# Performance work log

Measured on AMD Instinct MI355X. Metric: run time of the kernel, lower is better.

## Reference

```python
import jax, jax.numpy as jnp
import numpy as np

N_EMBD = 2048
QKV_EMBD = 2048
N_HEAD = 32
N_KV_HEAD = 8
HEAD_DIM = QKV_EMBD // N_HEAD  # 64
GROUPS = N_HEAD // N_KV_HEAD   # 4
ROPE_THETA = 10000.0
SCALE = float(np.sqrt(HEAD_DIM))


def setup_inputs() -> dict:
    key = jax.random.key(0)
    ks = jax.random.split(key, 12)
    B, S = 2, 2048
    inp = {
        "query": jax.random.normal(ks[0], (B, S, N_EMBD), jnp.float32),
        "key": jax.random.normal(ks[1], (B, S, N_EMBD), jnp.float32),
        "value": jax.random.normal(ks[2], (B, S, N_EMBD), jnp.float32),
        "mask": jnp.ones((B, S), dtype=bool),
        "Wq": jax.random.normal(ks[3], (QKV_EMBD, N_EMBD), jnp.float32) * 0.02,
        "bq": jnp.zeros((QKV_EMBD,), jnp.float32),
        "Wk": jax.random.normal(ks[4], (N_KV_HEAD * HEAD_DIM, N_EMBD), jnp.float32) * 0.02,
        "bk": jnp.zeros((N_KV_HEAD * HEAD_DIM,), jnp.float32),
        "Wv": jax.random.normal(ks[5], (N_KV_HEAD * HEAD_DIM, N_EMBD), jnp.float32) * 0.02,
        "bv": jnp.zeros((N_KV_HEAD * HEAD_DIM,), jnp.float32),
        "Wo": jax.random.normal(ks[6], (N_EMBD, QKV_EMBD), jnp.float32) * 0.02,
        "bo": jnp.zeros((N_EMBD,), jnp.float32),
    }
    return inp


def _rotate_half(x):
    d = x.shape[-1] // 2
    return jnp.concatenate([-x[..., d:], x[..., :d]], axis=-1)


def _rope_cos_sin(seq_len, dtype):
    # rope_factor == 1.0 -> no NTK adjustment; is_causal -> position_ids = arange
    inv_freq = 1.0 / (ROPE_THETA ** (jnp.arange(0, HEAD_DIM, 2, dtype=jnp.float32) / HEAD_DIM))
    pos = jnp.arange(seq_len, dtype=jnp.float32)
    freqs = jnp.einsum("i,j->ij", pos, inv_freq)           # [S, D/2]
    emb = jnp.concatenate([freqs, freqs], axis=-1)          # [S, D]
    return jnp.cos(emb).astype(dtype)[None, None], jnp.sin(emb).astype(dtype)[None, None]


def reference(query, key, value, mask, Wq, bq, Wk, bk, Wv, bv, Wo, bo):
    B, S, _ = query.shape
    Q = (query @ Wq.T + bq).reshape(B, S, N_HEAD, HEAD_DIM).transpose(0, 2, 1, 3)      # [B,H,S,D]
    K = (key @ Wk.T + bk).reshape(B, S, N_KV_HEAD, HEAD_DIM).transpose(0, 2, 1, 3)     # [B,KV,S,D]
    V = (value @ Wv.T + bv).reshape(B, S, N_KV_HEAD, HEAD_DIM).transpose(0, 2, 1, 3)

    cos, sin = _rope_cos_sin(S, Q.dtype)
    Q = Q * cos + _rotate_half(Q) * sin
    K = K * cos + _rotate_half(K) * sin

    # interleaved GQA repeat: each kv head serves GROUPS consecutive query heads
    K = jnp.repeat(K, GROUPS, axis=1)  # [B,H,S,D]
    V = jnp.repeat(V, GROUPS, axis=1)

    attn = jnp.einsum("bhqd,bhkd->bhqk", Q, K)              # [B,H,S,S]
    causal = jnp.tril(jnp.ones((S, S), dtype=bool))
    full_mask = mask[:, None, None, :] & causal[None, None]  # [B,1,S,S]
    attn = jnp.where(full_mask, attn, jnp.finfo(attn.dtype).min)
    attn_weights = jax.nn.softmax(attn / SCALE, axis=-1)     # dropout p=0 (eval)
    out = jnp.einsum("bhqk,bhkd->bhqd", attn_weights, V)
    out = out.transpose(0, 2, 1, 3).reshape(B, S, QKV_EMBD)
    return out @ Wo.T + bo
```

## Files before the change

### kernel.cpp

```cpp
#include <hip/hip_runtime.h>
#include <hip/hip_bf16.h>
#include <cmath>

#define NE   2048
#define NH   32
#define NKV  8
#define HD   64
#define SEQ  2048
#define NB   2

typedef __attribute__((ext_vector_type(4))) float f32x4;
typedef __attribute__((ext_vector_type(16))) float f32x16;
typedef __attribute__((ext_vector_type(8))) short bf16x8;
typedef __attribute__((ext_vector_type(4))) short bf16x4;

typedef const __attribute__((address_space(1))) void cgvoid;
typedef __attribute__((address_space(3))) void lvoid;

#define QSCALE 0.18033688011112042f

__device__ __forceinline__ short f2bf(float f) {
  union { float f; unsigned u; } v; v.f = f;
  unsigned r = v.u + 0x7fffu + ((v.u >> 16) & 1u);
  return (short)(r >> 16);
}

__device__ __forceinline__ unsigned cvt_pk_bf16(float a, float b) {
  unsigned r;
  asm("v_cvt_pk_bf16_f32 %0, %1, %2" : "=v"(r) : "v"(a), "v"(b));
  return r;
}

__global__ __launch_bounds__(256) void cvt_all(
    const float* __restrict__ s0, short* __restrict__ d0,
    const float* __restrict__ s1, short* __restrict__ d1,
    const float* __restrict__ s2, short* __restrict__ d2,
    const float* __restrict__ s3, short* __restrict__ d3,
    const float* __restrict__ s4, short* __restrict__ d4,
    const float* __restrict__ s5, short* __restrict__ d5,
    const float* __restrict__ s6, short* __restrict__ d6)
{
  int idx = blockIdx.x * 256 + threadIdx.x;
  const float* s; short* d; int rel;
  if      (idx < 1048576) { s = s0; d = d0; rel = idx; }
  else if (idx < 2097152) { s = s1; d = d1; rel = idx - 1048576; }
  else if (idx < 3145728) { s = s2; d = d2; rel = idx - 2097152; }
  else if (idx < 3670016) { s = s3; d = d3; rel = idx - 3145728; }
  else if (idx < 3801088) { s = s4; d = d4; rel = idx - 3670016; }
  else if (idx < 3932160) { s = s5; d = d5; rel = idx - 3801088; }
  else                    { s = s6; d = d6; rel = idx - 3932160; }
  size_t off = (size_t)rel * 8;
  f32x4 a = *(const f32x4*)(s + off);
  f32x4 b = *(const f32x4*)(s + off + 4);
  bf16x8 o;
  #pragma unroll
  for (int j = 0; j < 4; ++j) { o[j] = f2bf(a[j]); o[4 + j] = f2bf(b[j]); }
  *(bf16x8*)(d + off) = o;
}

template<int EPI>
__device__ __forceinline__ void gemm_body(
    short* As, short* Ws, int m0, int n0,
    const short* __restrict__ A, const short* __restrict__ W,
    const float* __restrict__ bias, void* __restrict__ Cout,
    int N, int K)
{
  const int t = threadIdx.x, lane = t & 63, w = t >> 6;
  const int lr = lane & 15, lg = lane >> 4;
  const int wm = (w >> 1) * 64, wn = (w & 1) * 64;

  const int sr = t >> 2, sc = (t & 3) * 8;
  const short* gA0 = A + (size_t)(m0 + sr) * K + sc;
  const short* gA1 = A + (size_t)(m0 + 64 + sr) * K + sc;
  const short* gW0 = W + (size_t)(n0 + sr) * K + sc;
  const short* gW1 = W + (size_t)(n0 + 64 + sr) * K + sc;
  short* lA0 = As + t * 8;
  short* lA1 = As + 2048 + t * 8;
  short* lW0 = Ws + t * 8;
  short* lW1 = Ws + 2048 + t * 8;

  f32x4 acc[4][4];
  #pragma unroll
  for (int i = 0; i < 4; ++i)
    #pragma unroll
    for (int j = 0; j < 4; ++j) acc[i][j] = (f32x4){0.f, 0.f, 0.f, 0.f};

  for (int k0 = 0; k0 < K; k0 += 32) {
    __builtin_amdgcn_global_load_lds((cgvoid*)(gA0 + k0), (lvoid*)lA0, 16, 0, 0);
    __builtin_amdgcn_global_load_lds((cgvoid*)(gA1 + k0), (lvoid*)lA1, 16, 0, 0);
    __builtin_amdgcn_global_load_lds((cgvoid*)(gW0 + k0), (lvoid*)lW0, 16, 0, 0);
    __builtin_amdgcn_global_load_lds((cgvoid*)(gW1 + k0), (lvoid*)lW1, 16, 0, 0);
    __syncthreads();
    bf16x8 af[4], wf[4];
    #pragma unroll
    for (int mf = 0; mf < 4; ++mf)
      af[mf] = *(const bf16x8*)(As + (wm + mf * 16 + lr) * 32 + lg * 8);
    #pragma unroll
    for (int nf = 0; nf < 4; ++nf)
      wf[nf] = *(const bf16x8*)(Ws + (wn + nf * 16 + lr) * 32 + lg * 8);
    #pragma unroll
    for (int mf = 0; mf < 4; ++mf)
      #pragma unroll
      for (int nf = 0; nf < 4; ++nf)
        acc[mf][nf] = __builtin_amdgcn_mfma_f32_16x16x32_bf16(af[mf], wf[nf], acc[mf][nf], 0, 0, 0);
    __syncthreads();
  }

  if (EPI == 0) {
    float* C = (float*)Cout;
    #pragma unroll
    for (int mf = 0; mf < 4; ++mf)
      #pragma unroll
      for (int nf = 0; nf < 4; ++nf)
        #pragma unroll
        for (int i = 0; i < 4; ++i) {
          int m = m0 + wm + mf * 16 + lg * 4 + i;
          int n = n0 + wn + nf * 16 + lr;
          C[(size_t)m * N + n] = acc[mf][nf][i] + bias[n];
        }
  } else if (EPI == 1) {
    short* C = (short*)Cout;
    #pragma unroll
    for (int mf = 0; mf < 4; ++mf)
      #pragma unroll
      for (int nf = 0; nf < 4; ++nf) {
        int n = n0 + wn + nf * 16 + lr;
        int kv = n >> 6, d = n & 63;
        int mb = m0 + wm + mf * 16 + lg * 4;
        int b = mb >> 11, s = mb & (SEQ - 1);
        bf16x4 pb;
        #pragma unroll
        for (int i = 0; i < 4; ++i) pb[i] = f2bf(acc[mf][nf][i] + bias[n]);
        *(bf16x4*)(C + (((size_t)b * NKV + kv) * HD + d) * SEQ + s) = pb;
      }
  } else {
    const int HN = (EPI == 2) ? NH : NKV;
    short* C = (short*)Cout;
    #pragma unroll
    for (int mf = 0; mf < 4; ++mf)
      #pragma unroll
      for (int nf2 = 0; nf2 < 2; ++nf2)
        #pragma unroll
        for (int i = 0; i < 4; ++i) {
          int m = m0 + wm + mf * 16 + lg * 4 + i;
          int b = m >> 11, s = m & (SEQ - 1);
          int n1 = n0 + wn + nf2 * 16 + lr;
          int n2 = n1 + 32;
          float v1 = acc[mf][nf2][i] + bias[n1];
          float v2 = acc[mf][nf2 + 2][i] + bias[n2];
          int d1 = n1 & 63;
          float inv = exp2f(-(float)d1 * (13.287712379549449f / 32.0f));
          float ang = (float)s * inv;
          float c, sn;
          __sincosf(ang, &sn, &c);
          float o1 = v1 * c - v2 * sn;
          float o2 = v2 * c + v1 * sn;
          if (EPI == 2) { o1 *= QSCALE; o2 *= QSCALE; }
          int h = n1 >> 6;
          size_t base = (((size_t)b * HN + h) * SEQ + s) * HD;
          C[base + d1]      = f2bf(o1);
          C[base + d1 + 32] = f2bf(o2);
        }
  }
}

template<int EPI>
__global__ __launch_bounds__(256) void gemm_bf16(
    const short* __restrict__ A, const short* __restrict__ W,
    const float* __restrict__ bias, void* __restrict__ Cout, int N, int K)
{
  __shared__ __align__(16) short As[128 * 32];
  __shared__ __align__(16) short Ws[128 * 32];
  gemm_body<EPI>(As, Ws, blockIdx.x * 128, blockIdx.y * 128, A, W, bias, Cout, N, K);
}

__global__ __launch_bounds__(256) void gemm_qkv(
    const short* __restrict__ qA, const short* __restrict__ Wq,
    const float* __restrict__ bq, short* __restrict__ Qout,
    const short* __restrict__ kA, const short* __restrict__ Wk,
    const float* __restrict__ bk, short* __restrict__ Kout,
    const short* __restrict__ vA, const short* __restrict__ Wv,
    const float* __restrict__ bv, short* __restrict__ Vout)
{
  __shared__ __align__(16) short As[128 * 32];
  __shared__ __align__(16) short Ws[128 * 32];
  int bid = blockIdx.x;
  if (bid < 512) {
    gemm_body<2>(As, Ws, (bid & 31) * 128, (bid >> 5) * 128, qA, Wq, bq, (void*)Qout, NE, NE);
  } else if (bid < 640) {
    int b2 = bid - 512;
    gemm_body<3>(As, Ws, (b2 & 31) * 128, (b2 >> 5) * 128, kA, Wk, bk, (void*)Kout, NKV * HD, NE);
  } else {
    int b2 = bid - 640;
    gemm_body<1>(As, Ws, (b2 & 31) * 128, (b2 >> 5) * 128, vA, Wv, bv, (void*)Vout, NKV * HD, NE);
  }
}

__global__ __launch_bounds__(256) void attn_kernel(
    const short* __restrict__ Q, const short* __restrict__ K,
    const short* __restrict__ Vt, short* __restrict__ O)
{
  __shared__ __align__(16) short Ks[2][64 * 64];
  __shared__ __align__(16) short Vs[2][64 * 64];

  const int t = threadIdx.x, lane = t & 63, w = t >> 6;
  const int l31 = lane & 31, hi = lane >> 5;
  const int by = blockIdx.y;
  const int b = by >> 3, kvh = by & 7;
  const int h = kvh * 4 + w;

  const short* Qh = Q + ((size_t)b * NH + h) * SEQ * HD;
  const short* Kh = K + ((size_t)b * NKV + kvh) * SEQ * HD;
  const short* Vh = Vt + ((size_t)b * NKV + kvh) * (size_t)HD * SEQ;

  #pragma unroll 1
  for (int pass = 0; pass < 2; ++pass) {
    const int qb32 = pass ? blockIdx.x : (63 - blockIdx.x);
    const int q0 = qb32 * 32;
    const int ntile = (qb32 >> 1) + 1;
    const int qpos = q0 + l31;

    bf16x8 qfr[4];
    #pragma unroll
    for (int dd = 0; dd < 4; ++dd)
      qfr[dd] = *(const bf16x8*)(Qh + (size_t)(q0 + l31) * HD + dd * 16 + hi * 8);

    f32x16 o[2];
    #pragma unroll
    for (int dh = 0; dh < 2; ++dh)
      #pragma unroll
      for (int r = 0; r < 16; ++r) o[dh][r] = 0.f;
    float lsum = 0.f;

    #pragma unroll
    for (int it = 0; it < 2; ++it) {
      int cid = it * 256 + t;
      int r = cid >> 3, c = cid & 7;
      int cs = ((c ^ (r & 7)) << 3);
      __builtin_amdgcn_global_load_lds((cgvoid*)(Kh + (size_t)r * HD + cs),
                                       (lvoid*)(Ks[0] + cid * 8), 16, 0, 0);
      __builtin_amdgcn_global_load_lds((cgvoid*)(Vh + (size_t)r * SEQ + cs),
                                       (lvoid*)(Vs[0] + cid * 8), 16, 0, 0);
    }
    __syncthreads();

    for (int ti = 0; ti < ntile; ++ti) {
      const int cur = ti & 1;
      if (ti + 1 < ntile) {
        const int kvn = (ti + 1) * 64;
        #pragma unroll
        for (int it = 0; it < 2; ++it) {
          int cid = it * 256 + t;
          int r = cid >> 3, c = cid & 7;
          int cs = ((c ^ (r & 7)) << 3);
          __builtin_amdgcn_global_load_lds((cgvoid*)(Kh + (size_t)(kvn + r) * HD + cs),
                                           (lvoid*)(Ks[cur ^ 1] + cid * 8), 16, 0, 0);
          __builtin_amdgcn_global_load_lds((cgvoid*)(Vh + (size_t)r * SEQ + kvn + cs),
                                           (lvoid*)(Vs[cur ^ 1] + cid * 8), 16, 0, 0);
        }
      }
      const int kv0 = ti * 64;
      const short* Kb = Ks[cur];
      const short* Vb = Vs[cur];

      f32x16 p[2];
      __builtin_amdgcn_s_setprio(1);
      #pragma unroll
      for (int f = 0; f < 2; ++f) {
        f32x16 z;
        #pragma unroll
        for (int r = 0; r < 16; ++r) z[r] = 0.f;
        #pragma unroll
        for (int dd = 0; dd < 4; ++dd) {
          int row = f * 32 + l31;
          bf16x8 ka = *(const bf16x8*)(Kb + row * 64 + (((2 * dd + hi) ^ (row & 7)) << 3));
          z = __builtin_amdgcn_mfma_f32_32x32x16_bf16(ka, qfr[dd], z, 0, 0, 0);
        }
        p[f] = z;
      }
      __builtin_amdgcn_s_setprio(0);

      if (ti == ntile - 1) {
        #pragma unroll
        for (int f = 0; f < 2; ++f)
          #pragma unroll
          for (int r = 0; r < 16; ++r) {
            int kpos = kv0 + f * 32 + (r & 3) + 8 * (r >> 2) + 4 * hi;
            if (kpos > qpos) p[f][r] = -INFINITY;
          }
      }

      unsigned pa[4][4];
      #pragma unroll
      for (int f = 0; f < 2; ++f) {
        float e[16];
        #pragma unroll
        for (int r = 0; r < 16; ++r) {
          e[r] = __builtin_amdgcn_exp2f(p[f][r]);
          lsum += e[r];
        }
        unsigned c[8];
        #pragma unroll
        for (int i = 0; i < 8; ++i) c[i] = cvt_pk_bf16(e[2 * i], e[2 * i + 1]);
        asm volatile("v_permlane32_swap_b32 %0, %1" : "+v"(c[0]), "+v"(c[2]));
        asm volatile("v_permlane32_swap_b32 %0, %1" : "+v"(c[1]), "+v"(c[3]));
        asm volatile("v_permlane32_swap_b32 %0, %1" : "+v"(c[4]), "+v"(c[6]));
        asm volatile("v_permlane32_swap_b32 %0, %1" : "+v"(c[5]), "+v"(c[7]));
        pa[2 * f][0] = c[0]; pa[2 * f][1] = c[1]; pa[2 * f][2] = c[2]; pa[2 * f][3] = c[3];
        pa[2 * f + 1][0] = c[4]; pa[2 * f + 1][1] = c[5];
        pa[2 * f + 1][2] = c[6]; pa[2 * f + 1][3] = c[7];
      }

      __builtin_amdgcn_s_setprio(1);
      #pragma unroll
      for (int ks = 0; ks < 4; ++ks) {
        bf16x8 paf = *(const bf16x8*)&pa[ks][0];
        #pragma unroll
        for (int dh = 0; dh < 2; ++dh) {
          int row = dh * 32 + l31;
          bf16x8 vb = *(const bf16x8*)(Vb + row * 64 + (((2 * ks + hi) ^ (row & 7)) << 3));
          o[dh] = __builtin_amdgcn_mfma_f32_32x32x16_bf16(paf, vb, o[dh], 0, 0, 0);
        }
      }
      __builtin_amdgcn_s_setprio(0);
      __syncthreads();
    }

    lsum += __shfl_xor(lsum, 32);
    #pragma unroll
    for (int r = 0; r < 16; ++r) {
      int crow = (r & 3) + 8 * (r >> 2) + 4 * hi;
      float li = __shfl(lsum, crow, 64);
      float invl = 1.0f / li;
      int s = q0 + crow;
      size_t base = (((size_t)b * SEQ + s) * NH + h) * HD;
      O[base + l31]      = f2bf(o[0][r] * invl);
      O[base + 32 + l31] = f2bf(o[1][r] * invl);
    }
  }
}

extern "C" void kernel_launch(void* const* d_in, const int* in_sizes, int n_in,
                              void* d_out, int out_size, void* d_ws, size_t ws_size,
                              hipStream_t stream) {
  (void)in_sizes; (void)n_in; (void)out_size; (void)ws_size;
  const float* q  = (const float*)d_in[0];
  const float* k  = (const float*)d_in[1];
  const float* v  = (const float*)d_in[2];
  const float* Wq = (const float*)d_in[4];
  const float* bq = (const float*)d_in[5];
  const float* Wk = (const float*)d_in[6];
  const float* bk = (const float*)d_in[7];
  const float* Wv = (const float*)d_in[8];
  const float* bv = (const float*)d_in[9];
  const float* Wo = (const float*)d_in[10];
  const float* bo = (const float*)d_in[11];

  const size_t SQ2 = (size_t)NB * SEQ * NE;
  const size_t W1  = (size_t)NE * NE;
  const size_t W2  = (size_t)(NKV * HD) * NE;
  const size_t KVN = (size_t)NB * NKV * SEQ * HD;

  short* ws = (short*)d_ws;
  short* qb  = ws;
  short* kb  = ws + SQ2;
  short* vb  = ws + 2 * SQ2;
  short* Wqb = ws + 3 * SQ2;
  short* Wkb = Wqb + W1;
  short* Wvb = Wkb + W2;
  short* Wob = Wvb + W2;
  short* Qr  = Wob + W1;
  short* Kr  = Qr + SQ2;
  short* Vr  = Kr + KVN;
  short* Ob  = qb;

  dim3 blk(256);

  cvt_all<<<17408, blk, 0, stream>>>(q, qb, k, kb, v, vb, Wq, Wqb, Wk, Wkb, Wv, Wvb, Wo, Wob);
  gemm_qkv<<<768, blk, 0, stream>>>(qb, Wqb, bq, Qr, kb, Wkb, bk, Kr, vb, Wvb, bv, Vr);
  attn_kernel<<<dim3(32, NB * NKV), blk, 0, stream>>>(Qr, Kr, Vr, Ob);
  gemm_bf16<0><<<dim3(32, 16), blk, 0, stream>>>(Ob, Wob, bo, d_out, NE, NE);
}
```

Baseline: 226.4 us.

## Double-buffer GEMM LDS tiles with K=64 steps and XOR-swizzled layout

Reworks the shared GEMM body so it prefetches the next K=64 tile into a second LDS buffer via global_load_lds while computing the current one, using explicit vmcnt waits and raw barriers. The LDS layout is XOR-swizzled by row to reduce bank conflicts on fragment reads, and MFMA sections raise wave priority. This hides global load latency and halves the barrier count per K, at the cost of 4x LDS per block (64KB), which may reduce occupancy.

```diff
diff --git a/kernel.cpp b/kernel.cpp
--- a/kernel.cpp
+++ b/kernel.cpp
@@ -69,41 +69,72 @@
   const int lr = lane & 15, lg = lane >> 4;
   const int wm = (w >> 1) * 64, wn = (w & 1) * 64;
 
-  const int sr = t >> 2, sc = (t & 3) * 8;
-  const short* gA0 = A + (size_t)(m0 + sr) * K + sc;
-  const short* gA1 = A + (size_t)(m0 + 64 + sr) * K + sc;
-  const short* gW0 = W + (size_t)(n0 + sr) * K + sc;
-  const short* gW1 = W + (size_t)(n0 + 64 + sr) * K + sc;
-  short* lA0 = As + t * 8;
-  short* lA1 = As + 2048 + t * 8;
-  short* lW0 = Ws + t * 8;
-  short* lW1 = Ws + 2048 + t * 8;
-
   f32x4 acc[4][4];
   #pragma unroll
   for (int i = 0; i < 4; ++i)
     #pragma unroll
     for (int j = 0; j < 4; ++j) acc[i][j] = (f32x4){0.f, 0.f, 0.f, 0.f};
 
-  for (int k0 = 0; k0 < K; k0 += 32) {
-    __builtin_amdgcn_global_load_lds((cgvoid*)(gA0 + k0), (lvoid*)lA0, 16, 0, 0);
-    __builtin_amdgcn_global_load_lds((cgvoid*)(gA1 + k0), (lvoid*)lA1, 16, 0, 0);
-    __builtin_amdgcn_global_load_lds((cgvoid*)(gW0 + k0), (lvoid*)lW0, 16, 0, 0);
-    __builtin_amdgcn_global_load_lds((cgvoid*)(gW1 + k0), (lvoid*)lW1, 16, 0, 0);
-    __syncthreads();
-    bf16x8 af[4], wf[4];
-    #pragma unroll
-    for (int mf = 0; mf < 4; ++mf)
-      af[mf] = *(const bf16x8*)(As + (wm + mf * 16 + lr) * 32 + lg * 8);
-    #pragma unroll
-    for (int nf = 0; nf < 4; ++nf)
-      wf[nf] = *(const bf16x8*)(Ws + (wn + nf * 16 + lr) * 32 + lg * 8);
-    #pragma unroll
-    for (int mf = 0; mf < 4; ++mf)
-      #pragma unroll
-      for (int nf = 0; nf < 4; ++nf)
-        acc[mf][nf] = __builtin_amdgcn_mfma_f32_16x16x32_bf16(af[mf], wf[nf], acc[mf][nf], 0, 0, 0);
-    __syncthreads();
+  const int nt = K >> 6;
+
+  #pragma unroll
+  for (int it = 0; it < 4; ++it) {
+    int e = it * 256 + t, r = e >> 3, c = e & 7;
+    int cs = ((c ^ (r & 7)) << 3);
+    __builtin_amdgcn_global_load_lds((cgvoid*)(A + (size_t)(m0 + r) * K + cs),
+                                     (lvoid*)(As + e * 8), 16, 0, 0);
+    __builtin_amdgcn_global_load_lds((cgvoid*)(W + (size_t)(n0 + r) * K + cs),
+                                     (lvoid*)(Ws + e * 8), 16, 0, 0);
+  }
+
+  for (int ti = 0; ti < nt; ++ti) {
+    const int cur = ti & 1;
+    const short* Ab = As + cur * 8192;
+    const short* Wb = Ws + cur * 8192;
+    if (ti + 1 < nt) {
+      const int k0 = (ti + 1) << 6;
+      short* An = As + (cur ^ 1) * 8192;
+      short* Wn = Ws + (cur ^ 1) * 8192;
+      #pragma unroll
+      for (int it = 0; it < 4; ++it) {
+        int e = it * 256 + t, r = e >> 3, c = e & 7;
+        int cs = ((c ^ (r & 7)) << 3);
+        __builtin_amdgcn_global_load_lds((cgvoid*)(A + (size_t)(m0 + r) * K + k0 + cs),
+                                         (lvoid*)(An + e * 8), 16, 0, 0);
+        __builtin_amdgcn_global_load_lds((cgvoid*)(W + (size_t)(n0 + r) * K + k0 + cs),
+                                         (lvoid*)(Wn + e * 8), 16, 0, 0);
+      }
+      asm volatile("s_waitcnt vmcnt(8)" ::: "memory");
+    } else {
+      asm volatile("s_waitcnt vmcnt(0)" ::: "memory");
+    }
+    __builtin_amdgcn_s_barrier();
+
+    bf16x8 af[2][4], wf[2][4];
+    #pragma unroll
+    for (int ks = 0; ks < 2; ++ks)
+      #pragma unroll
+      for (int mf = 0; mf < 4; ++mf) {
+        int row = wm + mf * 16 + lr;
+        af[ks][mf] = *(const bf16x8*)(Ab + row * 64 + (((ks * 4 + lg) ^ (row & 7)) << 3));
+      }
+    #pragma unroll
+    for (int ks = 0; ks < 2; ++ks)
+      #pragma unroll
+      for (int nf = 0; nf < 4; ++nf) {
+        int row = wn + nf * 16 + lr;
+        wf[ks][nf] = *(const bf16x8*)(Wb + row * 64 + (((ks * 4 + lg) ^ (row & 7)) << 3));
+      }
+    __builtin_amdgcn_s_setprio(1);
+    #pragma unroll
+    for (int ks = 0; ks < 2; ++ks)
+      #pragma unroll
+      for (int mf = 0; mf < 4; ++mf)
+        #pragma unroll
+        for (int nf = 0; nf < 4; ++nf)
+          acc[mf][nf] = __builtin_amdgcn_mfma_f32_16x16x32_bf16(af[ks][mf], wf[ks][nf], acc[mf][nf], 0, 0, 0);
+    __builtin_amdgcn_s_setprio(0);
+    __builtin_amdgcn_s_barrier();
   }
 
   if (EPI == 0) {
@@ -169,8 +200,8 @@
     const short* __restrict__ A, const short* __restrict__ W,
     const float* __restrict__ bias, void* __restrict__ Cout, int N, int K)
 {
-  __shared__ __align__(16) short As[128 * 32];
-  __shared__ __align__(16) short Ws[128 * 32];
+  __shared__ __align__(16) short As[2 * 128 * 64];
+  __shared__ __align__(16) short Ws[2 * 128 * 64];
   gemm_body<EPI>(As, Ws, blockIdx.x * 128, blockIdx.y * 128, A, W, bias, Cout, N, K);
 }
 
@@ -182,8 +213,8 @@
     const short* __restrict__ vA, const short* __restrict__ Wv,
     const float* __restrict__ bv, short* __restrict__ Vout)
 {
-  __shared__ __align__(16) short As[128 * 32];
-  __shared__ __align__(16) short Ws[128 * 32];
+  __shared__ __align__(16) short As[2 * 128 * 64];
+  __shared__ __align__(16) short Ws[2 * 128 * 64];
   int bid = blockIdx.x;
   if (bid < 512) {
     gemm_body<2>(As, Ws, (bid & 31) * 128, (bid >> 5) * 128, qA, Wq, bq, (void*)Qout, NE, NE);
```

Result: faster. 216.1 us (-4.6%).
